# Kernel optimization log

Measured on AMD Instinct MI355X. Metric: run time of the kernel, lower is better.

Reference implementation:

```python
import jax, jax.numpy as jnp
import numpy as np

B, S, H, NH = 2, 2048, 512, 8
DK = H // NH


def setup_inputs() -> dict:
    key = jax.random.key(0)
    ks = jax.random.split(key, 12)
    inp = {
        "query": jax.random.normal(ks[0], (B, S, H), dtype=jnp.float32),
        "key": jax.random.normal(ks[1], (B, S, H), dtype=jnp.float32),
        "value": jax.random.normal(ks[2], (B, S, H), dtype=jnp.float32),
        "bias": jax.random.normal(ks[3], (B, 1, S, S), dtype=jnp.float32),
        "mask": jax.random.randint(ks[4], (B, S), 0, 2, dtype=jnp.int32),
        "Wq": jax.random.normal(ks[5], (H, H), dtype=jnp.float32) * 0.02,
        "bq": jax.random.normal(ks[6], (H,), dtype=jnp.float32) * 0.02,
        "Wk": jax.random.normal(ks[7], (H, H), dtype=jnp.float32) * 0.02,
        "bk": jax.random.normal(ks[8], (H,), dtype=jnp.float32) * 0.02,
        "Wv": jax.random.normal(ks[9], (H, H), dtype=jnp.float32) * 0.02,
        "bv": jax.random.normal(ks[10], (H,), dtype=jnp.float32) * 0.02,
    }
    return inp


def reference(query, key, value, bias, mask, Wq, bq, Wk, bk, Wv, bv):
    b = query.shape[0]
    # torch nn.Linear: x @ W.T + b, then split heads -> [B, h, S, d_k]
    def proj(x, W, bb):
        y = x @ W.T + bb
        return y.reshape(b, -1, NH, DK).transpose(0, 2, 1, 3)

    q = proj(query, Wq, bq)
    k = proj(key, Wk, bk)
    v = proj(value, Wv, bv)

    score = jnp.einsum("bhqd,bhkd->bhqk", q, k) / np.sqrt(DK).astype(np.float32)
    # NOTE: the source swaps bias/mask when calling attention():
    #   the 0/1 mask is ADDED to the scores...
    mask_add = mask.reshape(b, 1, 1, -1).astype(score.dtype)
    score = score + mask_add
    #   ...and the float bias is used for the masked_fill (bias == 0 -> -1e30).
    score = jnp.where(bias == 0, jnp.asarray(-1e30, score.dtype), score)
    attn = jax.nn.softmax(score, axis=-1)  # dropout=None in the source call
    x = jnp.einsum("bhqk,bhkd->bhqd", attn, v)
    return x.transpose(0, 2, 1, 3).reshape(b, -1, NH * DK)
```

## Files before the change

### kernel.cpp

```cpp
#include <hip/hip_runtime.h>
#include <hip/hip_bf16.h>
#include <stdint.h>

#define B_  2
#define S_  2048
#define H_  512
#define NH_ 8
#define DK_ 64

typedef __bf16 bf16x8 __attribute__((ext_vector_type(8)));
typedef short  s16x4  __attribute__((ext_vector_type(4)));
typedef float  f32x4  __attribute__((ext_vector_type(4)));

static __device__ __forceinline__ uint32_t pk2(float a, float b) {
  __hip_bfloat162 h = __float22bfloat162_rn(float2{a, b});
  uint32_t u;
  __builtin_memcpy(&u, &h, 4);
  return u;
}

static __device__ __forceinline__ f32x4 mfma_k16(s16x4 a, s16x4 b, f32x4 c) {
#if defined(__HIP_DEVICE_COMPILE__)
  return __builtin_amdgcn_mfma_f32_16x16x16bf16_1k(a, b, c, 0, 0, 0);
#else
  (void)a; (void)b;
  return c;
#endif
}

typedef const __attribute__((address_space(1))) uint32_t* gas_t;
typedef __attribute__((address_space(3))) uint32_t* las_t;
static __device__ __forceinline__ void cp16(const void* g, void* l) {
  __builtin_amdgcn_global_load_lds((gas_t)g, (las_t)l, 16, 0, 0);
}

struct ProjArgs {
  const float* X[3];
  const float* W[3];
  const float* Bv[3];
  uint16_t*    O[3];
  const float* bias;
  const int*   mask;
  uint32_t*    zrow;
  float*       fmL;
};

__global__ __launch_bounds__(256) void prep_proj_kernel(ProjArgs pa) {
  __shared__ __align__(16) char psm[24640];
  int bid = blockIdx.x, t = threadIdx.x;

  if (bid >= 768) {
    if (bid < 1280) {
      int rr = bid - 768;
      const float* base = pa.bias + (size_t)rr * 8 * 2048 + t * 8;
      uint4 a[8], b2[8];
#pragma unroll
      for (int i = 0; i < 8; i++) {
        const uint4* src = (const uint4*)(base + (size_t)i * 2048);
        a[i] = src[0]; b2[i] = src[1];
      }
      uint32_t (*wbuf)[4] = (uint32_t (*)[4])psm;
      int wv = t >> 6, ln = t & 63;
#pragma unroll
      for (int i = 0; i < 8; i++) {
        bool z = ((a[i].x << 1) == 0u) | ((a[i].y << 1) == 0u) |
                 ((a[i].z << 1) == 0u) | ((a[i].w << 1) == 0u) |
                 ((b2[i].x << 1) == 0u) | ((b2[i].y << 1) == 0u) |
                 ((b2[i].z << 1) == 0u) | ((b2[i].w << 1) == 0u);
        uint64_t m = __ballot(z);
        if (ln == 0) {
          uint32_t bits = 0;
#pragma unroll
          for (int c = 0; c < 8; c++)
            bits |= (uint32_t)(((m >> (8 * c)) & 0xFFull) != 0ull) << c;
          wbuf[i][wv] = bits;
        }
      }
      __syncthreads();
      if (t < 8)
        pa.zrow[rr * 8 + t] = wbuf[t][0] | (wbuf[t][1] << 8) |
                              (wbuf[t][2] << 16) | (wbuf[t][3] << 24);
    } else {
      const float LOG2E = 1.44269504088896340736f;
#pragma unroll
      for (int i = 0; i < 16; i++) {
        int idx = i * 256 + t;
        pa.fmL[idx] = (float)pa.mask[idx] * LOG2E;
      }
    }
    return;
  }

  int xcd = bid & 7, j = bid >> 3;
  int gi = ((j >> 3) << 3) | xcd;
  int dtile = j & 7;
  int mat = gi >> 5, mtile = gi & 31;
  int m0 = mtile * 128, n0 = dtile * 64;
  const float* X  = pa.X[mat];
  const float* Wt = pa.W[mat];
  const float* Bv = pa.Bv[mat];
  uint16_t*    O  = pa.O[mat];

  uint16_t (*Xs)[64] = (uint16_t (*)[64])psm;
  uint16_t (*Ws)[64] = (uint16_t (*)[64])(psm + 16384);

  int w = t >> 6, l = t & 63, lo = l & 15, g = l >> 4;
  int lr = l >> 4;
  int lc = l & 15;

  const float* Xp = X + (size_t)(m0 + w * 32 + lr) * 512 + lc * 4;
  const float* Wp = Wt + (size_t)(n0 + w * 16 + lr) * 512 + lc * 4;

  f32x4 acc[2][4];
#pragma unroll
  for (int st = 0; st < 2; st++)
#pragma unroll
    for (int dt = 0; dt < 4; dt++) acc[st][dt] = (f32x4){0.f, 0.f, 0.f, 0.f};

  float4 xa[8], wa2[4];
#pragma unroll
  for (int i = 0; i < 8; i++) xa[i] = *(const float4*)(Xp + (size_t)i * 4 * 512);
#pragma unroll
  for (int i = 0; i < 4; i++) wa2[i] = *(const float4*)(Wp + (size_t)i * 4 * 512);

  for (int kb = 0; kb < 8; kb++) {
#pragma unroll
    for (int i = 0; i < 8; i++) {
      int r = w * 32 + i * 4 + lr;
      int s0 = (lc >> 1) ^ (r & 7);
      uint2 pk{pk2(xa[i].x, xa[i].y), pk2(xa[i].z, xa[i].w)};
      *(uint2*)&Xs[r][s0 * 8 + (lc & 1) * 4] = pk;
    }
#pragma unroll
    for (int i = 0; i < 4; i++) {
      int r = w * 16 + i * 4 + lr;
      int s0 = (lc >> 1) ^ (r & 7);
      uint2 pk{pk2(wa2[i].x, wa2[i].y), pk2(wa2[i].z, wa2[i].w)};
      *(uint2*)&Ws[r][s0 * 8 + (lc & 1) * 4] = pk;
    }
    __syncthreads();
    if (kb < 7) {
      const float* Xn = Xp + (kb + 1) * 64;
      const float* Wn = Wp + (kb + 1) * 64;
#pragma unroll
      for (int i = 0; i < 8; i++) xa[i] = *(const float4*)(Xn + (size_t)i * 4 * 512);
#pragma unroll
      for (int i = 0; i < 4; i++) wa2[i] = *(const float4*)(Wn + (size_t)i * 4 * 512);
    }
#pragma unroll
    for (int kk = 0; kk < 2; kk++) {
      int seg = (kk * 4 + g) ^ (lo & 7);
      bf16x8 xf[2], wf[4];
#pragma unroll
      for (int st = 0; st < 2; st++)
        xf[st] = *(const bf16x8*)&Xs[w * 32 + st * 16 + lo][seg * 8];
#pragma unroll
      for (int dt = 0; dt < 4; dt++)
        wf[dt] = *(const bf16x8*)&Ws[dt * 16 + lo][seg * 8];
      if (mat < 2) {
#pragma unroll
        for (int st = 0; st < 2; st++)
#pragma unroll
          for (int dt = 0; dt < 4; dt++)
            acc[st][dt] = __builtin_amdgcn_mfma_f32_16x16x32_bf16(wf[dt], xf[st], acc[st][dt], 0, 0, 0);
      } else {
#pragma unroll
        for (int st = 0; st < 2; st++)
#pragma unroll
          for (int dt = 0; dt < 4; dt++)
            acc[st][dt] = __builtin_amdgcn_mfma_f32_16x16x32_bf16(xf[st], wf[dt], acc[st][dt], 0, 0, 0);
      }
    }
    __syncthreads();
  }

  if (mat < 2) {
    float scale = (mat == 0) ? 0.125f : 1.0f;
    float4 bv4[4];
#pragma unroll
    for (int dt = 0; dt < 4; dt++)
      bv4[dt] = *(const float4*)(Bv + n0 + dt * 16 + g * 4);
#pragma unroll
    for (int st = 0; st < 2; st++) {
      int ss = m0 + w * 32 + st * 16 + lo;
      int bb = ss >> 11, sIn = ss & 2047;
      uint16_t* obase = O + ((size_t)(bb * NH_ + dtile) * S_ + sIn) * DK_;
#pragma unroll
      for (int dt = 0; dt < 4; dt++) {
        float v0 = (acc[st][dt][0] + bv4[dt].x) * scale;
        float v1 = (acc[st][dt][1] + bv4[dt].y) * scale;
        float v2 = (acc[st][dt][2] + bv4[dt].z) * scale;
        float v3 = (acc[st][dt][3] + bv4[dt].w) * scale;
        uint2 pk{pk2(v0, v1), pk2(v2, v3)};
        *(uint2*)(obase + dt * 16 + g * 4) = pk;
      }
    }
  } else {
    float bval[4];
#pragma unroll
    for (int dt = 0; dt < 4; dt++) bval[dt] = Bv[n0 + dt * 16 + lo];
#pragma unroll
    for (int st = 0; st < 2; st++) {
      int m = m0 + w * 32 + st * 16 + g * 4;
      int bb = m >> 11, sIn = m & 2047;
#pragma unroll
      for (int dt = 0; dt < 4; dt++) {
        int dd = dt * 16 + lo;
        float v0 = acc[st][dt][0] + bval[dt];
        float v1 = acc[st][dt][1] + bval[dt];
        float v2 = acc[st][dt][2] + bval[dt];
        float v3 = acc[st][dt][3] + bval[dt];
        uint2 pk{pk2(v0, v1), pk2(v2, v3)};
        *(uint2*)(O + ((size_t)(bb * NH_ + dtile) * DK_ + dd) * S_ + sIn) = pk;
      }
    }
  }
}

__global__ __launch_bounds__(256, 2) void attn_kernel(
    const uint16_t* __restrict__ Qb, const uint16_t* __restrict__ Kb,
    const uint16_t* __restrict__ Vt, const uint32_t* __restrict__ zrow,
    const float* __restrict__ fmL, const float* __restrict__ bias,
    float* __restrict__ out) {
  int bid = blockIdx.x;
  int bh = bid & 15, qtile = bid >> 4;
  int b = bh >> 3, h = bh & 7;
  int q0 = qtile * 32;
  int t = threadIdx.x;
  int w = t >> 6, l = t & 63, lo = l & 15, g = l >> 4;

  __shared__ __align__(16) char smem[32768];
  uint16_t* KsB = (uint16_t*)smem;
  uint16_t* VsB = (uint16_t*)(smem + 16384);

  const uint16_t* Qh = Qb + (size_t)bh * S_ * DK_;
  const uint16_t* Kh = Kb + (size_t)bh * S_ * DK_;
  const uint16_t* Vh = Vt + (size_t)bh * DK_ * S_;

  int lrow = l >> 3, lseg = (l & 7) ^ lrow;
  const uint16_t* kbase = Kh + (size_t)(w * 16 + lrow) * DK_ + lseg * 8;
  const uint16_t* vbase = Vh + (size_t)(w * 16 + lrow) * S_ + lseg * 8;
  uint16_t* kd0 = KsB + (w * 16) * 64;
  uint16_t* kd8 = KsB + (w * 16 + 8) * 64;
  uint16_t* vd0 = VsB + (w * 16) * 64;
  uint16_t* vd8 = VsB + (w * 16 + 8) * 64;

  uint32_t zall = zrow[(b << 11) + q0 + (l & 31)];
#pragma unroll
  for (int s = 1; s < 32; s <<= 1) zall |= __shfl_xor(zall, s);

  bf16x8 qf[2][2];
#pragma unroll
  for (int qt = 0; qt < 2; qt++)
#pragma unroll
    for (int kk = 0; kk < 2; kk++)
      qf[qt][kk] = *(const bf16x8*)(Qh + (size_t)(q0 + qt * 16 + lo) * DK_ + kk * 32 + g * 8);

  f32x4 o[4][2];
#pragma unroll
  for (int dt = 0; dt < 4; dt++)
#pragma unroll
    for (int qt = 0; qt < 2; qt++) o[dt][qt] = (f32x4){0.f, 0.f, 0.f, 0.f};
  float ts[2] = {0.f, 0.f};

  const float* fmrow = fmL + b * S_ + w * 16 + g * 4;
  const float LOG2E = 1.44269504088896340736f;

  cp16(kbase, kd0);
  cp16(kbase + 512, kd8);
  cp16(vbase, vd0);
  cp16(vbase + 8 * S_, vd8);

  for (int kb = 0; kb < 32; kb++) {
    int cur = kb & 1;
    int k0 = kb * 64;
    float4 mv4 = *(const float4*)(fmrow + k0);
    __syncthreads();
    if (kb + 1 < 32) {
      int kn = k0 + 64;
      int nb = (cur ^ 1) * 4096;
      cp16(kbase + (size_t)kn * 64, kd0 + nb);
      cp16(kbase + (size_t)kn * 64 + 512, kd8 + nb);
      cp16(vbase + kn, vd0 + nb);
      cp16(vbase + kn + 8 * S_, vd8 + nb);
    }
    const uint16_t* KsT = KsB + cur * 4096;
    const uint16_t* VsT = VsB + cur * 4096;

    s16x4 vf[4];
    {
      int s = (2 * w + (g >> 1)) ^ (lo & 7);
      int off = s * 8 + (g & 1) * 4;
#pragma unroll
      for (int dt = 0; dt < 4; dt++)
        vf[dt] = *(const s16x4*)(VsT + (dt * 16 + lo) * 64 + off);
    }
    bf16x8 kf[2];
#pragma unroll
    for (int kk = 0; kk < 2; kk++) {
      int s = (kk * 4 + g) ^ (lo & 7);
      kf[kk] = *(const bf16x8*)(KsT + (w * 16 + lo) * 64 + s * 8);
    }

    f32x4 c[2];
#pragma unroll
    for (int qt = 0; qt < 2; qt++) {
      f32x4 z = {0.f, 0.f, 0.f, 0.f};
      z = __builtin_amdgcn_mfma_f32_16x16x32_bf16(kf[0], qf[qt][0], z, 0, 0, 0);
      c[qt] = __builtin_amdgcn_mfma_f32_16x16x32_bf16(kf[1], qf[qt][1], z, 0, 0, 0);
    }

    float p[2][4];
    if (((zall >> kb) & 1u) == 0u) {
#pragma unroll
      for (int qt = 0; qt < 2; qt++) {
        p[qt][0] = __builtin_amdgcn_exp2f(__builtin_fmaf(c[qt][0], LOG2E, mv4.x));
        p[qt][1] = __builtin_amdgcn_exp2f(__builtin_fmaf(c[qt][1], LOG2E, mv4.y));
        p[qt][2] = __builtin_amdgcn_exp2f(__builtin_fmaf(c[qt][2], LOG2E, mv4.z));
        p[qt][3] = __builtin_amdgcn_exp2f(__builtin_fmaf(c[qt][3], LOG2E, mv4.w));
      }
    } else {
#pragma unroll
      for (int qt = 0; qt < 2; qt++) {
        float4 bz = *(const float4*)(bias + ((size_t)(b * S_ + q0 + qt * 16 + lo)) * S_ + k0 + w * 16 + g * 4);
        p[qt][0] = (bz.x == 0.f) ? 0.f : __builtin_amdgcn_exp2f(__builtin_fmaf(c[qt][0], LOG2E, mv4.x));
        p[qt][1] = (bz.y == 0.f) ? 0.f : __builtin_amdgcn_exp2f(__builtin_fmaf(c[qt][1], LOG2E, mv4.y));
        p[qt][2] = (bz.z == 0.f) ? 0.f : __builtin_amdgcn_exp2f(__builtin_fmaf(c[qt][2], LOG2E, mv4.z));
        p[qt][3] = (bz.w == 0.f) ? 0.f : __builtin_amdgcn_exp2f(__builtin_fmaf(c[qt][3], LOG2E, mv4.w));
      }
    }

    s16x4 pf[2];
#pragma unroll
    for (int qt = 0; qt < 2; qt++) {
      ts[qt] += (p[qt][0] + p[qt][1]) + (p[qt][2] + p[qt][3]);
      union { s16x4 v; uint32_t u[2]; } uu;
      uu.u[0] = pk2(p[qt][0], p[qt][1]);
      uu.u[1] = pk2(p[qt][2], p[qt][3]);
      pf[qt] = uu.v;
    }

#pragma unroll
    for (int dt = 0; dt < 4; dt++)
#pragma unroll
      for (int qt = 0; qt < 2; qt++)
        o[dt][qt] = mfma_k16(vf[dt], pf[qt], o[dt][qt]);
  }

  float* OT = (float*)smem;
  float* LS = (float*)(smem + 8448);
#pragma unroll
  for (int qt = 0; qt < 2; qt++) {
    float v = ts[qt];
    v += __shfl_xor(v, 16);
    v += __shfl_xor(v, 32);
    ts[qt] = v;
  }
  __syncthreads();
  if (g == 0) {
#pragma unroll
    for (int qt = 0; qt < 2; qt++) LS[(w * 2 + qt) * 16 + lo] = ts[qt];
  }
#pragma unroll
  for (int ww = 0; ww < 4; ww++) {
    if (w == ww) {
#pragma unroll
      for (int dt = 0; dt < 4; dt++)
#pragma unroll
        for (int qt = 0; qt < 2; qt++)
#pragma unroll
          for (int r = 0; r < 4; r++) {
            int idx = (dt * 16 + g * 4 + r) * 33 + qt * 16 + lo;
            if (ww == 0) OT[idx] = o[dt][qt][r];
            else         OT[idx] += o[dt][qt][r];
          }
    }
    __syncthreads();
  }
  {
    int q = t >> 3, dseg = (t & 7) * 8;
    int qt2 = q >> 4, lo2 = q & 15;
    float lsum = LS[(0 * 2 + qt2) * 16 + lo2] + LS[(1 * 2 + qt2) * 16 + lo2] +
                 LS[(2 * 2 + qt2) * 16 + lo2] + LS[(3 * 2 + qt2) * 16 + lo2];
    float linv = 1.0f / fmaxf(lsum, 1e-30f);
    float* ob = out + ((size_t)(b * S_ + q0 + q)) * H_ + h * DK_ + dseg;
#pragma unroll
    for (int i = 0; i < 2; i++) {
      float4 v;
      v.x = OT[(dseg + i * 4 + 0) * 33 + q] * linv;
      v.y = OT[(dseg + i * 4 + 1) * 33 + q] * linv;
      v.z = OT[(dseg + i * 4 + 2) * 33 + q] * linv;
      v.w = OT[(dseg + i * 4 + 3) * 33 + q] * linv;
      *(float4*)(ob + i * 4) = v;
    }
  }
}

extern "C" void kernel_launch(void* const* d_in, const int* in_sizes, int n_in,
                              void* d_out, int out_size, void* d_ws, size_t ws_size,
                              hipStream_t stream) {
  const float* query = (const float*)d_in[0];
  const float* key   = (const float*)d_in[1];
  const float* value = (const float*)d_in[2];
  const float* bias  = (const float*)d_in[3];
  const int*   mask  = (const int*)d_in[4];
  const float* Wq = (const float*)d_in[5];
  const float* bq = (const float*)d_in[6];
  const float* Wk = (const float*)d_in[7];
  const float* bk = (const float*)d_in[8];
  const float* Wv = (const float*)d_in[9];
  const float* bv = (const float*)d_in[10];

  char* ws = (char*)d_ws;
  uint32_t* zrow = (uint32_t*)ws;
  float*    fmL  = (float*)(ws + 16384);
  uint16_t* Qb = (uint16_t*)(ws + (size_t)(1 << 20));
  uint16_t* Kb = (uint16_t*)(ws + (size_t)(5 << 20));
  uint16_t* Vt = (uint16_t*)(ws + (size_t)(9 << 20));

  ProjArgs pa;
  pa.X[0] = query; pa.X[1] = key; pa.X[2] = value;
  pa.W[0] = Wq;    pa.W[1] = Wk;  pa.W[2] = Wv;
  pa.Bv[0] = bq;   pa.Bv[1] = bk; pa.Bv[2] = bv;
  pa.O[0] = Qb;    pa.O[1] = Kb;  pa.O[2] = Vt;
  pa.bias = bias;  pa.mask = mask;
  pa.zrow = zrow;  pa.fmL = fmL;

  prep_proj_kernel<<<1281, 256, 0, stream>>>(pa);

  attn_kernel<<<1024, 256, 0, stream>>>(Qb, Kb, Vt, zrow, fmL, bias, (float*)d_out);
}
```

Before: 157.6 us.

## Give each wave private double-buffered K/V staging and drop per-iteration block barrier

Each wave now stages only the 16 keys it consumes, K rows plus the matching V columns, into its own 8 KB slice of LDS with double buffering. The per-iteration __syncthreads is replaced by explicit vmcnt waits, and the additive-mask row is prefetched one iteration ahead. This removes block-wide synchronisation and cross-wave stalls in the key loop and simplifies the V addressing. It relies on hand-counted outstanding-load counts, which could break if the compiler reorders loads. The launch bounds also drop the two-blocks-per-CU minimum, which changes the register budget.

```diff
diff --git a/kernel.cpp b/kernel.cpp
--- a/kernel.cpp
+++ b/kernel.cpp
@@ -217,7 +217,7 @@
   }
 }
 
-__global__ __launch_bounds__(256, 2) void attn_kernel(
+__global__ __launch_bounds__(256) void attn_kernel(
     const uint16_t* __restrict__ Qb, const uint16_t* __restrict__ Kb,
     const uint16_t* __restrict__ Vt, const uint32_t* __restrict__ zrow,
     const float* __restrict__ fmL, const float* __restrict__ bias,
@@ -230,8 +230,7 @@
   int w = t >> 6, l = t & 63, lo = l & 15, g = l >> 4;
 
   __shared__ __align__(16) char smem[32768];
-  uint16_t* KsB = (uint16_t*)smem;
-  uint16_t* VsB = (uint16_t*)(smem + 16384);
+  char* wq = smem + w * 8192;
 
   const uint16_t* Qh = Qb + (size_t)bh * S_ * DK_;
   const uint16_t* Kh = Kb + (size_t)bh * S_ * DK_;
@@ -239,11 +238,17 @@
 
   int lrow = l >> 3, lseg = (l & 7) ^ lrow;
   const uint16_t* kbase = Kh + (size_t)(w * 16 + lrow) * DK_ + lseg * 8;
-  const uint16_t* vbase = Vh + (size_t)(w * 16 + lrow) * S_ + lseg * 8;
-  uint16_t* kd0 = KsB + (w * 16) * 64;
-  uint16_t* kd8 = KsB + (w * 16 + 8) * 64;
-  uint16_t* vd0 = VsB + (w * 16) * 64;
-  uint16_t* vd8 = VsB + (w * 16 + 8) * 64;
+  const uint16_t* vbase = Vh + (size_t)(l >> 1) * S_ + w * 16 + (l & 1) * 8;
+
+  auto stage = [&](int kb, int buf) {
+    char* dst = wq + buf * 4096;
+    const uint16_t* ksrc = kbase + ((size_t)kb << 12);
+    cp16(ksrc, dst);
+    cp16(ksrc + 8 * DK_, dst + 1024);
+    const uint16_t* vsrc = vbase + kb * 64;
+    cp16(vsrc, dst + 2048);
+    cp16(vsrc + (size_t)32 * S_, dst + 3072);
+  };
 
   uint32_t zall = zrow[(b << 11) + q0 + (l & 31)];
 #pragma unroll
@@ -266,40 +271,35 @@
   const float* fmrow = fmL + b * S_ + w * 16 + g * 4;
   const float LOG2E = 1.44269504088896340736f;
 
-  cp16(kbase, kd0);
-  cp16(kbase + 512, kd8);
-  cp16(vbase, vd0);
-  cp16(vbase + 8 * S_, vd8);
+  stage(0, 0);
+  float4 mvc = *(const float4*)(fmrow);
+  float4 mvn = mvc;
 
   for (int kb = 0; kb < 32; kb++) {
     int cur = kb & 1;
     int k0 = kb * 64;
-    float4 mv4 = *(const float4*)(fmrow + k0);
-    __syncthreads();
     if (kb + 1 < 32) {
-      int kn = k0 + 64;
-      int nb = (cur ^ 1) * 4096;
-      cp16(kbase + (size_t)kn * 64, kd0 + nb);
-      cp16(kbase + (size_t)kn * 64 + 512, kd8 + nb);
-      cp16(vbase + kn, vd0 + nb);
-      cp16(vbase + kn + 8 * S_, vd8 + nb);
-    }
-    const uint16_t* KsT = KsB + cur * 4096;
-    const uint16_t* VsT = VsB + cur * 4096;
+      stage(kb + 1, cur ^ 1);
+      mvn = *(const float4*)(fmrow + k0 + 64);
+      asm volatile("s_waitcnt vmcnt(5)" ::: "memory");
+    } else {
+      asm volatile("s_waitcnt vmcnt(0)" ::: "memory");
+    }
+    __builtin_amdgcn_sched_barrier(0);
+
+    const uint16_t* KsT = (const uint16_t*)(wq + cur * 4096);
+    const uint16_t* VsT = (const uint16_t*)(wq + cur * 4096 + 2048);
 
     s16x4 vf[4];
-    {
-      int s = (2 * w + (g >> 1)) ^ (lo & 7);
-      int off = s * 8 + (g & 1) * 4;
-#pragma unroll
-      for (int dt = 0; dt < 4; dt++)
-        vf[dt] = *(const s16x4*)(VsT + (dt * 16 + lo) * 64 + off);
-    }
+#pragma unroll
+    for (int dt = 0; dt < 4; dt++)
+      vf[dt] = *(const s16x4*)(VsT + (dt * 16 + lo) * 16 + g * 4);
+
     bf16x8 kf[2];
 #pragma unroll
     for (int kk = 0; kk < 2; kk++) {
       int s = (kk * 4 + g) ^ (lo & 7);
-      kf[kk] = *(const bf16x8*)(KsT + (w * 16 + lo) * 64 + s * 8);
+      kf[kk] = *(const bf16x8*)(KsT + lo * 64 + s * 8);
     }
 
     f32x4 c[2];
@@ -310,6 +310,7 @@
       c[qt] = __builtin_amdgcn_mfma_f32_16x16x32_bf16(kf[1], qf[qt][1], z, 0, 0, 0);
     }
 
+    float4 mv4 = mvc;
     float p[2][4];
     if (((zall >> kb) & 1u) == 0u) {
 #pragma unroll
@@ -345,6 +346,8 @@
 #pragma unroll
       for (int qt = 0; qt < 2; qt++)
         o[dt][qt] = mfma_k16(vf[dt], pf[qt], o[dt][qt]);
+
+    mvc = mvn;
   }
 
   float* OT = (float*)smem;
```

Measured after the change: 170.4 us. 8.1% more time.
